# Kernel optimization log

Hardware: AMD Instinct MI355X
Metric: run time of the kernel (lower is better)

## Reference

```python
import jax, jax.numpy as jnp
import numpy as np

B, T, D, H, O = 128, 2048, 128, 1024, 32
LAST = 20          # last_n_outputs
ALPHA = 0.9        # leak rate
SPARSITY = 0.8


def _make_w_r(rng):
    # Faithful to torch __init__: randn, /max, sparsify, /spectral radius
    w_r = rng.standard_normal((H, H))
    w_r = w_r / np.max(w_r)
    w_r = np.where(rng.random(w_r.shape) < SPARSITY, 0.0, w_r)
    max_abs_eig = np.max(np.abs(np.linalg.eigvals(w_r)))
    return (w_r / max_abs_eig).astype(np.float32)


def setup_inputs() -> dict:
    key = jax.random.key(0)
    k_x, k_in, k_w, k_b = jax.random.split(key, 4)
    rng = np.random.default_rng(0)
    x = jax.random.normal(k_x, (B, T, D), dtype=jnp.float32)
    w_in = jax.random.normal(k_in, (D, H), dtype=jnp.float32) * 0.2
    w_r = jnp.asarray(_make_w_r(rng))
    W = jax.random.normal(k_w, (H * LAST, O), dtype=jnp.float32) * 0.02
    b = jax.random.normal(k_b, (O,), dtype=jnp.float32) * 0.02
    return {"x": x, "w_in": w_in, "w_r": w_r, "W": W, "b": b}


def reference(x, w_in, w_r, W, b):
    # Precompute the non-recurrent term in one batched GEMM: [B,T,H]
    xw = jnp.einsum('btd,dh->bth', x, w_in)

    # t == 0: h0 = 0, and original code sets h = h_hat (no leaky mix)
    h = jnp.tanh(xw[:, 0])  # [B, H]

    def step(h, xt):
        h_hat = jnp.tanh(xt + h @ w_r)
        return (1.0 - ALPHA) * h + ALPHA * h_hat, None

    # steps 1 .. T-LAST-1 : no outputs collected
    xw_mid = jnp.swapaxes(xw[:, 1:T - LAST], 0, 1)   # [T-LAST-1, B, H]
    h, _ = jax.lax.scan(step, h, xw_mid)

    def step_out(h, xt):
        h_hat = jnp.tanh(xt + h @ w_r)
        h_new = (1.0 - ALPHA) * h + ALPHA * h_hat
        return h_new, h_new

    # last LAST steps: collect hidden states
    xw_tail = jnp.swapaxes(xw[:, T - LAST:], 0, 1)   # [LAST, B, H]
    _, hs = jax.lax.scan(step_out, h, xw_tail)       # [LAST, B, H]

    # concat in time order along feature dim -> [B, LAST*H]
    out_cat = jnp.transpose(hs, (1, 0, 2)).reshape(B, LAST * H)
    return out_cat @ W + b
```

## Files before the change

kernel.cpp:

```cpp
#include <hip/hip_runtime.h>
#include <stdint.h>
#include <stddef.h>

#define B_    128
#define T_    2048
#define D_    128
#define H_    1024
#define O_    32
#define LAST_ 20

#define NB_   8
#define NC_   16
#define RING_ 4
#define TWARM_ 8

typedef __bf16 bf16x8 __attribute__((ext_vector_type(8)));
typedef __bf16 bf16x4 __attribute__((ext_vector_type(4)));
typedef float  f32x4  __attribute__((ext_vector_type(4)));
typedef unsigned int u32x4 __attribute__((ext_vector_type(4)));

union Pack8  { unsigned long long u;    bf16x4 v; };
union Pack16 { unsigned long long u[2]; u32x4 d; bf16x8 v; };

__device__ __forceinline__ float tanh_fast(float s) {
    float a = fminf(fmaxf(s, -12.0f), 12.0f);
    float e = __expf(2.0f * a);
    return (e - 1.0f) / (e + 1.0f);
}

__global__ __launch_bounds__(256, 1) void esn_persist(
    const float* __restrict__ x, const float* __restrict__ w_in,
    const float* __restrict__ w_r, __bf16* __restrict__ h_exA,
    __bf16* __restrict__ h_exB, float* __restrict__ hs,
    int* __restrict__ flags)
{
    __shared__ bf16x8 ls[2][16][128];

    const int wg  = (int)blockIdx.x;
    const int bb  = wg & (NB_ - 1);
    const int cb  = wg >> 3;
    const int tid = (int)threadIdx.x;
    const int wv  = tid >> 6;
    const int ln  = tid & 63;
    const int nn  = ln & 15;
    const int q   = ln >> 4;
    const int b0  = bb * 16;
    const int n0  = cb * 64 + wv * 16;

    const unsigned long long tdead =
        __builtin_amdgcn_s_memrealtime() + 300000000ull;

    int xcc;
    asm volatile("s_getreg_b32 %0, hwreg(HW_REG_XCC_ID)" : "=s"(xcc));
    const int mytag = 0x5A5A0000 | (xcc & 0xFF);
    if (tid == 0)
        __hip_atomic_store(flags + wg, mytag, __ATOMIC_RELAXED,
                           __HIP_MEMORY_SCOPE_AGENT);

    bf16x8 win[4];
    #pragma unroll
    for (int c = 0; c < 4; ++c) {
        bf16x8 f;
        #pragma unroll
        for (int j = 0; j < 8; ++j)
            f[j] = (__bf16)w_in[(size_t)(c * 32 + q * 8 + j) * H_ + (n0 + nn)];
        win[c] = f;
    }
    bf16x8 wr[32];
    #pragma unroll
    for (int kc = 0; kc < 32; ++kc) {
        bf16x8 f;
        #pragma unroll
        for (int j = 0; j < 8; ++j)
            f[j] = (__bf16)w_r[(size_t)(kc * 32 + q * 8 + j) * H_ + (n0 + nn)];
        wr[kc] = f;
    }

    bool votefast;
    {
        int alleq = 0;
        for (;;) {
            int seen = 1; alleq = 1;
            #pragma unroll
            for (int k = 0; k < NC_; ++k) {
                int v = __hip_atomic_load(flags + (bb + 8 * k), __ATOMIC_RELAXED,
                                          __HIP_MEMORY_SCOPE_AGENT);
                seen  &= (int)((v & 0xFFFF0000) == 0x5A5A0000);
                alleq &= (int)(v == mytag);
            }
            if (seen) break;
            __builtin_amdgcn_s_sleep(8);
            if (__builtin_amdgcn_s_memrealtime() > tdead) { alleq = 0; break; }
        }
        votefast = (alleq != 0);
    }

    const float* xrow = x + (size_t)(b0 + nn) * T_ * D_ + q * 8;
    const size_t hrow = (size_t)(b0 + nn) * H_;

    const int scol = (ln >> 2) * 64 + (ln & 3) * 16 + 12;

    f32x4 xn[8];
    bf16x8 xf[4];
    {
        #pragma unroll
        for (int c = 0; c < 4; ++c) {
            xn[2 * c]     = *(const f32x4*)(xrow + c * 32);
            xn[2 * c + 1] = *(const f32x4*)(xrow + c * 32 + 4);
        }
        #pragma unroll
        for (int c = 0; c < 4; ++c) {
            bf16x8 f;
            #pragma unroll
            for (int j = 0; j < 4; ++j) {
                f[j]     = (__bf16)xn[2 * c][j];
                f[j + 4] = (__bf16)xn[2 * c + 1][j];
            }
            xf[c] = f;
        }
    }

    float hm0 = 0.f, hm1 = 0.f, hm2 = 0.f, hm3 = 0.f;

    for (int t = 0; t < T_; ++t) {
        {
            const int tn = (t + 1 < T_) ? t + 1 : T_ - 1;
            const float* xp = xrow + (size_t)tn * D_;
            #pragma unroll
            for (int c = 0; c < 4; ++c) {
                xn[2 * c]     = *(const f32x4*)(xp + c * 32);
                xn[2 * c + 1] = *(const f32x4*)(xp + c * 32 + 4);
            }
        }

        f32x4 acc[8];
        #pragma unroll
        for (int i = 0; i < 8; ++i) acc[i] = (f32x4){0.f, 0.f, 0.f, 0.f};

        #pragma unroll
        for (int c = 0; c < 4; ++c)
            acc[c] = __builtin_amdgcn_mfma_f32_16x16x32_bf16(win[c], xf[c], acc[c], 0, 0, 0);

        if (t > 0) {
            const unsigned long long want1 =
                (unsigned long long)((((t - 1) >> 2) & 1) ^ 1) * 0x100000001ull;
            const int sb = (t - 1) & 1;
            const size_t slotoff =
                (size_t)((t - 1) & (RING_ - 1)) * (B_ * H_) + (size_t)b0 * H_;
            Pack16 pk[8];

            if (votefast && t >= TWARM_) {
                {
                    const unsigned long long* sp = (const unsigned long long*)
                        (h_exA + slotoff + 15 * H_ + scol);
                    int spins = 0;
                    for (;;) {
                        unsigned long long s;
                        asm volatile("global_load_dwordx2 %0, %1, off sc0 nt"
                                     : "=v"(s) : "v"(sp) : "memory");
                        asm volatile("s_waitcnt vmcnt(0)" : "+v"(s) :: "memory");
                        if (__all(((s ^ want1) & 0x100000001ull) == 0)) break;
                        if (((++spins) & 255) == 0 &&
                            __builtin_amdgcn_s_memrealtime() > tdead) break;
                    }
                }
                {
                    int spins = 0;
                    for (;;) {
                        #pragma unroll
                        for (int i = 0; i < 8; ++i) {
                            const int p = wv * 512 + i * 64 + ln;
                            const __bf16* gp = h_exA + slotoff
                                + (size_t)(p >> 7) * H_ + (p & 127) * 8;
                            asm volatile("global_load_dwordx4 %0, %1, off sc0 nt"
                                         : "=v"(pk[i].d) : "v"(gp) : "memory");
                        }
                        asm volatile("s_waitcnt vmcnt(0)"
                                     : "+v"(pk[0].d), "+v"(pk[1].d), "+v"(pk[2].d),
                                       "+v"(pk[3].d), "+v"(pk[4].d), "+v"(pk[5].d),
                                       "+v"(pk[6].d), "+v"(pk[7].d) :: "memory");
                        __builtin_amdgcn_sched_barrier(0);
                        unsigned ok = 1u;
                        #pragma unroll
                        for (int i = 0; i < 8; ++i) {
                            ok &= (unsigned)(((pk[i].u[0] ^ want1) & 0x100000001ull) == 0);
                            ok &= (unsigned)(((pk[i].u[1] ^ want1) & 0x100000001ull) == 0);
                        }
                        if (__all(ok != 0u)) break;
                        if (((++spins) & 63) == 0 &&
                            __builtin_amdgcn_s_memrealtime() > tdead) break;
                    }
                }
            } else {
                const __bf16* hbase = h_exB + slotoff;
                int spins = 0;
                for (;;) {
                    #pragma unroll
                    for (int i = 0; i < 8; ++i) {
                        const int p = wv * 512 + i * 64 + ln;
                        const unsigned long long* gp = (const unsigned long long*)
                            (hbase + (size_t)(p >> 7) * H_ + (p & 127) * 8);
                        pk[i].u[0] = __hip_atomic_load(gp, __ATOMIC_RELAXED,
                                                       __HIP_MEMORY_SCOPE_AGENT);
                        pk[i].u[1] = __hip_atomic_load(gp + 1, __ATOMIC_RELAXED,
                                                       __HIP_MEMORY_SCOPE_AGENT);
                    }
                    unsigned ok = 1u;
                    #pragma unroll
                    for (int i = 0; i < 8; ++i) {
                        ok &= (unsigned)(((pk[i].u[0] ^ want1) & 0x100000001ull) == 0);
                        ok &= (unsigned)(((pk[i].u[1] ^ want1) & 0x100000001ull) == 0);
                    }
                    if (__all(ok != 0u)) break;
                    __builtin_amdgcn_s_sleep(1);
                    if (((++spins) & 63) == 0 &&
                        __builtin_amdgcn_s_memrealtime() > tdead) break;
                }
            }

            #pragma unroll
            for (int i = 0; i < 8; ++i) {
                const int p = wv * 512 + i * 64 + ln;
                const int r = p >> 7, ch = p & 127;
                ls[sb][r][ch ^ (r & 7)] = pk[i].v;
            }

            __syncthreads();

            #pragma unroll
            for (int kc = 0; kc < 32; ++kc) {
                bf16x8 a = ls[sb][nn][(kc * 4 + q) ^ (nn & 7)];
                acc[kc & 7] = __builtin_amdgcn_mfma_f32_16x16x32_bf16(wr[kc], a, acc[kc & 7], 0, 0, 0);
            }
        }

        const f32x4 asum = ((acc[0] + acc[4]) + (acc[1] + acc[5]))
                         + ((acc[2] + acc[6]) + (acc[3] + acc[7]));
        const float th0 = tanh_fast(asum[0]);
        const float th1 = tanh_fast(asum[1]);
        const float th2 = tanh_fast(asum[2]);
        const float th3 = tanh_fast(asum[3]);
        if (t == 0) {
            hm0 = th0; hm1 = th1; hm2 = th2; hm3 = th3;
        } else {
            hm0 = 0.1f * hm0 + 0.9f * th0;
            hm1 = 0.1f * hm1 + 0.9f * th1;
            hm2 = 0.1f * hm2 + 0.9f * th2;
            hm3 = 0.1f * hm3 + 0.9f * th3;
        }

        {
            Pack8 p;
            p.v = (bf16x4){(__bf16)hm0, (__bf16)hm1, (__bf16)hm2, (__bf16)hm3};
            const unsigned long long tg =
                (unsigned long long)(((t >> 2) & 1) ^ 1) * 0x100000001ull;
            p.u = (p.u & ~0x100000001ull) | tg;
            const size_t poff = (size_t)(t & (RING_ - 1)) * (B_ * H_)
                                + hrow + n0 + q * 4;
            if (votefast) {
                unsigned long long* opA = (unsigned long long*)(h_exA + poff);
                asm volatile("global_store_dwordx2 %0, %1, off sc0"
                             :: "v"(opA), "v"(p.u) : "memory");
                if (t < TWARM_) {
                    unsigned long long* opB = (unsigned long long*)(h_exB + poff);
                    __hip_atomic_store(opB, p.u, __ATOMIC_RELAXED,
                                       __HIP_MEMORY_SCOPE_AGENT);
                }
            } else {
                unsigned long long* opB = (unsigned long long*)(h_exB + poff);
                __hip_atomic_store(opB, p.u, __ATOMIC_RELAXED,
                                   __HIP_MEMORY_SCOPE_AGENT);
            }
        }

        if (t >= T_ - LAST_) {
            f32x4* sp = (f32x4*)(hs + (size_t)(t - (T_ - LAST_)) * (B_ * H_)
                                    + hrow + n0 + q * 4);
            *sp = (f32x4){hm0, hm1, hm2, hm3};
        }
        #pragma unroll
        for (int c = 0; c < 4; ++c) {
            bf16x8 f;
            #pragma unroll
            for (int j = 0; j < 4; ++j) {
                f[j]     = (__bf16)xn[2 * c][j];
                f[j + 4] = (__bf16)xn[2 * c + 1][j];
            }
            xf[c] = f;
        }
    }
}

__global__ __launch_bounds__(256) void esn_out(
    const float* __restrict__ hs, const float* __restrict__ Wm,
    const float* __restrict__ bias, float* __restrict__ out)
{
    const int b   = (int)blockIdx.x;
    const int tid = (int)threadIdx.x;
    float acc[O_];
    #pragma unroll
    for (int o = 0; o < O_; ++o) acc[o] = 0.f;

    for (int k = tid; k < LAST_ * H_; k += 256) {
        const float hv = hs[(size_t)(k >> 10) * (B_ * H_) + (size_t)b * H_ + (k & (H_ - 1))];
        const f32x4* wp = (const f32x4*)(Wm + (size_t)k * O_);
        #pragma unroll
        for (int v = 0; v < 8; ++v) {
            f32x4 w4 = wp[v];
            acc[4 * v + 0] = fmaf(hv, w4[0], acc[4 * v + 0]);
            acc[4 * v + 1] = fmaf(hv, w4[1], acc[4 * v + 1]);
            acc[4 * v + 2] = fmaf(hv, w4[2], acc[4 * v + 2]);
            acc[4 * v + 3] = fmaf(hv, w4[3], acc[4 * v + 3]);
        }
    }

    __shared__ float red[256][O_ + 1];
    #pragma unroll
    for (int o = 0; o < O_; ++o) red[tid][o] = acc[o];
    __syncthreads();
    if (tid < O_) {
        float s = bias[tid];
        for (int i = 0; i < 256; ++i) s += red[i][tid];
        out[(size_t)b * O_ + tid] = s;
    }
}

extern "C" void kernel_launch(void* const* d_in, const int* in_sizes, int n_in,
                              void* d_out, int out_size, void* d_ws, size_t ws_size,
                              hipStream_t stream)
{
    const float* x    = (const float*)d_in[0];
    const float* w_in = (const float*)d_in[1];
    const float* w_r  = (const float*)d_in[2];
    const float* Wm   = (const float*)d_in[3];
    const float* bias = (const float*)d_in[4];
    float* out        = (float*)d_out;

    const size_t flag_bytes = 4096;
    const size_t ring_bytes = (size_t)RING_ * B_ * H_ * sizeof(__bf16);
    const size_t hs_bytes   = (size_t)LAST_ * B_ * H_ * sizeof(float);
    if (ws_size < flag_bytes + 2 * ring_bytes + hs_bytes) return;

    int*    flags = (int*)d_ws;
    __bf16* h_exA = (__bf16*)((char*)d_ws + flag_bytes);
    __bf16* h_exB = (__bf16*)((char*)d_ws + flag_bytes + ring_bytes);
    float*  hs    = (float*)((char*)d_ws + flag_bytes + 2 * ring_bytes);

    hipMemsetAsync(flags, 0x00, flag_bytes, stream);
    hipMemsetAsync(h_exA, 0xAA, 2 * ring_bytes, stream);

    hipLaunchKernelGGL(esn_persist, dim3(NB_ * NC_), dim3(256), 0, stream,
                       x, w_in, w_r, h_exA, h_exB, hs, flags);
    hipLaunchKernelGGL(esn_out, dim3(B_), dim3(256), 0, stream,
                       hs, Wm, bias, out);
}
```

Before: 6.197 ms.

## Split recurrent GEMM along K across waves with LDS reduction

Each wave now holds a K-slice of w_r covering all four 16-column output blocks of the workgroup. In the fast path it loads its own K-slice of h straight from global memory into registers, skipping the LDS staging and barrier. Partial sums from the four waves are then combined through a small double-buffered LDS reduction before tanh. This removes the LDS round trip for h and lets each wave start its MFMAs on its own data, at the cost of a barrier and an LDS reduction on every step.

```diff
diff --git a/kernel.cpp b/kernel.cpp
--- a/kernel.cpp
+++ b/kernel.cpp
@@ -35,6 +35,7 @@
     int* __restrict__ flags)
 {
     __shared__ bf16x8 ls[2][16][128];
+    __shared__ f32x4  lsr[2][4][64][5];
 
     const int wg  = (int)blockIdx.x;
     const int bb  = wg & (NB_ - 1);
@@ -66,14 +67,18 @@
             f[j] = (__bf16)w_in[(size_t)(c * 32 + q * 8 + j) * H_ + (n0 + nn)];
         win[c] = f;
     }
-    bf16x8 wr[32];
+    bf16x8 wrS[8][4];
     #pragma unroll
-    for (int kc = 0; kc < 32; ++kc) {
-        bf16x8 f;
-        #pragma unroll
-        for (int j = 0; j < 8; ++j)
-            f[j] = (__bf16)w_r[(size_t)(kc * 32 + q * 8 + j) * H_ + (n0 + nn)];
-        wr[kc] = f;
+    for (int kcl = 0; kcl < 8; ++kcl) {
+        #pragma unroll
+        for (int nb = 0; nb < 4; ++nb) {
+            bf16x8 f;
+            #pragma unroll
+            for (int j = 0; j < 8; ++j)
+                f[j] = (__bf16)w_r[(size_t)((wv * 8 + kcl) * 32 + q * 8 + j) * H_
+                                   + (cb * 64 + nb * 16 + nn)];
+            wrS[kcl][nb] = f;
+        }
     }
 
     bool votefast;
@@ -133,13 +138,15 @@
             }
         }
 
-        f32x4 acc[8];
-        #pragma unroll
-        for (int i = 0; i < 8; ++i) acc[i] = (f32x4){0.f, 0.f, 0.f, 0.f};
-
-        #pragma unroll
-        for (int c = 0; c < 4; ++c)
-            acc[c] = __builtin_amdgcn_mfma_f32_16x16x32_bf16(win[c], xf[c], acc[c], 0, 0, 0);
+        f32x4 xa0 = {0.f, 0.f, 0.f, 0.f}, xa1 = {0.f, 0.f, 0.f, 0.f};
+        xa0 = __builtin_amdgcn_mfma_f32_16x16x32_bf16(win[0], xf[0], xa0, 0, 0, 0);
+        xa1 = __builtin_amdgcn_mfma_f32_16x16x32_bf16(win[1], xf[1], xa1, 0, 0, 0);
+        xa0 = __builtin_amdgcn_mfma_f32_16x16x32_bf16(win[2], xf[2], xa0, 0, 0, 0);
+        xa1 = __builtin_amdgcn_mfma_f32_16x16x32_bf16(win[3], xf[3], xa1, 0, 0, 0);
+
+        f32x4 accp[4];
+        #pragma unroll
+        for (int nb = 0; nb < 4; ++nb) accp[nb] = (f32x4){0.f, 0.f, 0.f, 0.f};
 
         if (t > 0) {
             const unsigned long long want1 =
@@ -147,7 +154,6 @@
             const int sb = (t - 1) & 1;
             const size_t slotoff =
                 (size_t)((t - 1) & (RING_ - 1)) * (B_ * H_) + (size_t)b0 * H_;
-            Pack16 pk[8];
 
             if (votefast && t >= TWARM_) {
                 {
@@ -164,34 +170,42 @@
                             __builtin_amdgcn_s_memrealtime() > tdead) break;
                     }
                 }
-                {
-                    int spins = 0;
-                    for (;;) {
-                        #pragma unroll
-                        for (int i = 0; i < 8; ++i) {
-                            const int p = wv * 512 + i * 64 + ln;
-                            const __bf16* gp = h_exA + slotoff
-                                + (size_t)(p >> 7) * H_ + (p & 127) * 8;
-                            asm volatile("global_load_dwordx4 %0, %1, off sc0 nt"
-                                         : "=v"(pk[i].d) : "v"(gp) : "memory");
-                        }
-                        asm volatile("s_waitcnt vmcnt(0)"
-                                     : "+v"(pk[0].d), "+v"(pk[1].d), "+v"(pk[2].d),
-                                       "+v"(pk[3].d), "+v"(pk[4].d), "+v"(pk[5].d),
-                                       "+v"(pk[6].d), "+v"(pk[7].d) :: "memory");
-                        __builtin_amdgcn_sched_barrier(0);
-                        unsigned ok = 1u;
-                        #pragma unroll
-                        for (int i = 0; i < 8; ++i) {
-                            ok &= (unsigned)(((pk[i].u[0] ^ want1) & 0x100000001ull) == 0);
-                            ok &= (unsigned)(((pk[i].u[1] ^ want1) & 0x100000001ull) == 0);
-                        }
-                        if (__all(ok != 0u)) break;
-                        if (((++spins) & 63) == 0 &&
-                            __builtin_amdgcn_s_memrealtime() > tdead) break;
-                    }
+                Pack16 pk[8];
+                const __bf16* fb = h_exA + slotoff + (size_t)nn * H_
+                                   + (size_t)(wv * 256) + q * 8;
+                int spins = 0;
+                for (;;) {
+                    #pragma unroll
+                    for (int i = 0; i < 8; ++i) {
+                        const __bf16* gp = fb + (size_t)(i * 32);
+                        asm volatile("global_load_dwordx4 %0, %1, off sc0 nt"
+                                     : "=v"(pk[i].d) : "v"(gp) : "memory");
+                    }
+                    asm volatile("s_waitcnt vmcnt(0)"
+                                 : "+v"(pk[0].d), "+v"(pk[1].d), "+v"(pk[2].d),
+                                   "+v"(pk[3].d), "+v"(pk[4].d), "+v"(pk[5].d),
+                                   "+v"(pk[6].d), "+v"(pk[7].d) :: "memory");
+                    __builtin_amdgcn_sched_barrier(0);
+                    unsigned ok = 1u;
+                    #pragma unroll
+                    for (int i = 0; i < 8; ++i) {
+                        ok &= (unsigned)(((pk[i].u[0] ^ want1) & 0x100000001ull) == 0);
+                        ok &= (unsigned)(((pk[i].u[1] ^ want1) & 0x100000001ull) == 0);
+                    }
+                    if (__all(ok != 0u)) break;
+                    if (((++spins) & 63) == 0 &&
+                        __builtin_amdgcn_s_memrealtime() > tdead) break;
+                }
+                #pragma unroll
+                for (int kcl = 0; kcl < 8; ++kcl) {
+                    const bf16x8 fr = pk[kcl].v;
+                    accp[0] = __builtin_amdgcn_mfma_f32_16x16x32_bf16(wrS[kcl][0], fr, accp[0], 0, 0, 0);
+                    accp[1] = __builtin_amdgcn_mfma_f32_16x16x32_bf16(wrS[kcl][1], fr, accp[1], 0, 0, 0);
+                    accp[2] = __builtin_amdgcn_mfma_f32_16x16x32_bf16(wrS[kcl][2], fr, accp[2], 0, 0, 0);
+                    accp[3] = __builtin_amdgcn_mfma_f32_16x16x32_bf16(wrS[kcl][3], fr, accp[3], 0, 0, 0);
                 }
             } else {
+                Pack16 pk[8];
                 const __bf16* hbase = h_exB + slotoff;
                 int spins = 0;
                 for (;;) {
@@ -216,30 +230,38 @@
                     if (((++spins) & 63) == 0 &&
                         __builtin_amdgcn_s_memrealtime() > tdead) break;
                 }
-            }
-
-            #pragma unroll
-            for (int i = 0; i < 8; ++i) {
-                const int p = wv * 512 + i * 64 + ln;
-                const int r = p >> 7, ch = p & 127;
-                ls[sb][r][ch ^ (r & 7)] = pk[i].v;
-            }
-
-            __syncthreads();
-
-            #pragma unroll
-            for (int kc = 0; kc < 32; ++kc) {
-                bf16x8 a = ls[sb][nn][(kc * 4 + q) ^ (nn & 7)];
-                acc[kc & 7] = __builtin_amdgcn_mfma_f32_16x16x32_bf16(wr[kc], a, acc[kc & 7], 0, 0, 0);
-            }
-        }
-
-        const f32x4 asum = ((acc[0] + acc[4]) + (acc[1] + acc[5]))
-                         + ((acc[2] + acc[6]) + (acc[3] + acc[7]));
-        const float th0 = tanh_fast(asum[0]);
-        const float th1 = tanh_fast(asum[1]);
-        const float th2 = tanh_fast(asum[2]);
-        const float th3 = tanh_fast(asum[3]);
+                #pragma unroll
+                for (int i = 0; i < 8; ++i) {
+                    const int p = wv * 512 + i * 64 + ln;
+                    const int r = p >> 7, ch = p & 127;
+                    ls[sb][r][ch ^ (r & 7)] = pk[i].v;
+                }
+                __syncthreads();
+                #pragma unroll
+                for (int kcl = 0; kcl < 8; ++kcl) {
+                    const int kg = wv * 8 + kcl;
+                    const bf16x8 fr = ls[sb][nn][(kg * 4 + q) ^ (nn & 7)];
+                    accp[0] = __builtin_amdgcn_mfma_f32_16x16x32_bf16(wrS[kcl][0], fr, accp[0], 0, 0, 0);
+                    accp[1] = __builtin_amdgcn_mfma_f32_16x16x32_bf16(wrS[kcl][1], fr, accp[1], 0, 0, 0);
+                    accp[2] = __builtin_amdgcn_mfma_f32_16x16x32_bf16(wrS[kcl][2], fr, accp[2], 0, 0, 0);
+                    accp[3] = __builtin_amdgcn_mfma_f32_16x16x32_bf16(wrS[kcl][3], fr, accp[3], 0, 0, 0);
+                }
+            }
+        }
+
+        const int rb = t & 1;
+        #pragma unroll
+        for (int nb = 0; nb < 4; ++nb)
+            lsr[rb][wv][ln][nb] = accp[nb];
+        __syncthreads();
+        const f32x4 red = (lsr[rb][0][ln][wv] + lsr[rb][1][ln][wv])
+                        + (lsr[rb][2][ln][wv] + lsr[rb][3][ln][wv]);
+
+        const f32x4 val = (xa0 + xa1) + red;
+        const float th0 = tanh_fast(val[0]);
+        const float th1 = tanh_fast(val[1]);
+        const float th2 = tanh_fast(val[2]);
+        const float th3 = tanh_fast(val[3]);
         if (t == 0) {
             hm0 = th0; hm1 = th1; hm2 = th2; hm3 = th3;
         } else {
```

After: 6.725 ms. 1.09x slower.
